# Performance work log

Measured on AMD Instinct MI355X. Metric: run time of the kernel, lower is better.

Reference implementation:

```python
import jax, jax.numpy as jnp
import numpy as np

WH, WW = 16, 16
NUM_HEADS = 16
DIM = 1024
BATCH = 64
SEQ = WH * WW + 1  # 257, includes cls token
NUM_REL = (2 * WH - 1) * (2 * WW - 1) + 3  # 964


def _make_rel_pos_index(wh, ww):
    # BEiT relative position index construction (intended semantics of the torch code)
    coords = np.stack(np.meshgrid(np.arange(wh), np.arange(ww), indexing='ij'))  # [2, wh, ww]
    flat = coords.reshape(2, -1)  # [2, wh*ww]
    rel = flat[:, :, None] - flat[:, None, :]  # [2, N-1, N-1]
    rel = rel.transpose(1, 2, 0).astype(np.int64)
    rel[:, :, 0] += wh - 1
    rel[:, :, 1] += ww - 1
    rel[:, :, 0] *= 2 * ww - 1
    num_rel = (2 * wh - 1) * (2 * ww - 1) + 3
    idx = np.zeros((wh * ww + 1, wh * ww + 1), dtype=np.int32)
    idx[1:, 1:] = rel.sum(-1)
    idx[0, :] = num_rel - 3  # cls-to-token
    idx[:, 0] = num_rel - 2  # token-to-cls
    idx[0, 0] = num_rel - 1  # cls-to-cls
    return idx


def setup_inputs() -> dict:
    key = jax.random.key(0)
    ks = jax.random.split(key, 7)
    return {
        'x': jax.random.normal(ks[0], (BATCH, SEQ, DIM), dtype=jnp.float32),
        'qkv_weight': jax.random.normal(ks[1], (3 * DIM, DIM), dtype=jnp.float32) * 0.02,
        'query_bias': jax.random.normal(ks[2], (DIM,), dtype=jnp.float32) * 0.02,
        'value_bias': jax.random.normal(ks[3], (DIM,), dtype=jnp.float32) * 0.02,
        'rel_pos_bias_table': jax.random.normal(ks[4], (NUM_REL, NUM_HEADS), dtype=jnp.float32) * 0.02,
        'proj_weight': jax.random.normal(ks[5], (DIM, DIM), dtype=jnp.float32) * 0.02,
        'proj_bias': jax.random.normal(ks[6], (DIM,), dtype=jnp.float32) * 0.02,
        'rel_pos_index': jnp.asarray(_make_rel_pos_index(WH, WW)),
    }


def reference(x, qkv_weight, query_bias, value_bias, rel_pos_bias_table,
              proj_weight, proj_bias, rel_pos_index):
    B, N, C = x.shape
    H = rel_pos_bias_table.shape[-1]
    D = qkv_weight.shape[0] // 3 // H
    scale = D ** -0.5
    # qkv bias: (q_bias, zeros, v_bias) as in the torch module
    qkv_bias = jnp.concatenate([query_bias, jnp.zeros_like(value_bias), value_bias])
    qkv = x @ qkv_weight.T + qkv_bias  # [B, N, 3*H*D]
    qkv = qkv.reshape(B, N, 3, H, D).transpose(2, 0, 3, 1, 4)  # [3, B, H, N, D]
    q, k, v = qkv[0] * scale, qkv[1], qkv[2]
    attn = jnp.einsum('bhqd,bhkd->bhqk', q, k)  # [B, H, N, N]
    bias = rel_pos_bias_table[rel_pos_index]  # [N, N, H]
    attn = attn + bias.transpose(2, 0, 1)[None]  # add per-head bias
    attn = jax.nn.softmax(attn, axis=-1)
    out = jnp.einsum('bhqk,bhkd->bhqd', attn, v)  # [B, H, N, D]
    out = out.transpose(0, 2, 1, 3).reshape(B, N, H * D)
    return out @ proj_weight.T + proj_bias
```

## Files before the change

kernel.cpp:

```cpp
#include <hip/hip_runtime.h>


typedef unsigned short u16;
typedef __attribute__((ext_vector_type(8))) short bf16x8;
typedef __attribute__((ext_vector_type(4))) float f32x4;

#define MFMA16(a, b, c) __builtin_amdgcn_mfma_f32_16x16x32_bf16(a, b, c, 0, 0, 0)
#define GLDS16(g, l)                                                           \
  __builtin_amdgcn_global_load_lds(                                            \
      (const __attribute__((address_space(1))) void*)(g),                      \
      (__attribute__((address_space(3))) void*)(l), 16, 0, 0)

#define QOFF 0
#define KOFF 16842752
#define VTOFF 33685504
#define VTP 264

__device__ __forceinline__ u16 f2bf(float f) {
  unsigned u = __builtin_bit_cast(unsigned, f);
  u += 0x7FFFu + ((u >> 16) & 1u);
  return (u16)(u >> 16);
}

__global__ __launch_bounds__(256) void cvt_bf16(const float* __restrict__ in,
                                                u16* __restrict__ out, int n4) {
  int i = blockIdx.x * 256 + threadIdx.x;
  if (i < n4) {
    float4 v = ((const float4*)in)[i];
    uint2 o;
    o.x = (unsigned)f2bf(v.x) | ((unsigned)f2bf(v.y) << 16);
    o.y = (unsigned)f2bf(v.z) | ((unsigned)f2bf(v.w) << 16);
    ((uint2*)out)[i] = o;
  }
}

__global__ __launch_bounds__(256) void bias_pre(const float* __restrict__ tab,
                                                const int* __restrict__ idx,
                                                float* __restrict__ out) {
  int t = blockIdx.x * 256 + threadIdx.x;
  if (t < 66049) {
    int id = idx[t];
    const float* row = tab + (size_t)id * 16;
#pragma unroll
    for (int h = 0; h < 16; h++)
      out[(size_t)h * 66049 + t] = row[h] * 1.4426950408889634f;
  }
}


#define GEMM_PROLOG(M_, K_)                                                    \
  __shared__ __align__(16) u16 As[128 * 32];                                   \
  __shared__ __align__(16) u16 Bs[128 * 32];                                   \
  const int M = (M_), K = (K_);                                                \
  const int tid = threadIdx.x;                                                 \
  const int lane = tid & 63, wave = tid >> 6;                                  \
  const int quad = lane >> 4, l15 = lane & 15;                                 \
  const int wr = (wave >> 1) * 64, wc = (wave & 1) * 64;                       \
  const int m0 = blockIdx.y * 128, n0 = blockIdx.x * 128;                      \
  int ar0 = m0 + (tid >> 2); if (ar0 > M - 1) ar0 = M - 1;                     \
  int ar1 = m0 + 64 + (tid >> 2); if (ar1 > M - 1) ar1 = M - 1;                \
  const u16* pa0 = A + (size_t)ar0 * K + (tid & 3) * 8;                        \
  const u16* pa1 = A + (size_t)ar1 * K + (tid & 3) * 8;                        \
  const u16* pb0 = B + (size_t)(n0 + (tid >> 2)) * K + (tid & 3) * 8;          \
  const u16* pb1 = pb0 + (size_t)64 * K;                                       \
  f32x4 acc[4][4];                                                             \
  _Pragma("unroll") for (int i = 0; i < 4; i++)                                \
  _Pragma("unroll") for (int j = 0; j < 4; j++)                                \
      acc[i][j] = (f32x4){0.f, 0.f, 0.f, 0.f};                                 \
  for (int k0 = 0; k0 < K; k0 += 32) {                                         \
    __syncthreads();                                                           \
    GLDS16(pa0 + k0, As + tid * 8);                                            \
    GLDS16(pa1 + k0, As + 2048 + tid * 8);                                     \
    GLDS16(pb0 + k0, Bs + tid * 8);                                            \
    GLDS16(pb1 + k0, Bs + 2048 + tid * 8);                                     \
    __syncthreads();                                                           \
    bf16x8 af[4], bf[4];                                                       \
    _Pragma("unroll") for (int t = 0; t < 4; t++)                              \
        af[t] = *(const bf16x8*)(As + (wr + t * 16 + l15) * 32 + quad * 8);    \
    _Pragma("unroll") for (int t = 0; t < 4; t++)                              \
        bf[t] = *(const bf16x8*)(Bs + (wc + t * 16 + l15) * 32 + quad * 8);    \
    _Pragma("unroll") for (int i = 0; i < 4; i++)                              \
    _Pragma("unroll") for (int j = 0; j < 4; j++)                              \
        acc[i][j] = MFMA16(af[i], bf[j], acc[i][j]);                           \
  }

__global__ __launch_bounds__(256) void gemm_qkv(
    const u16* __restrict__ A, const u16* __restrict__ B,
    const float* __restrict__ qbias, const float* __restrict__ vbias,
    u16* __restrict__ C) {
  GEMM_PROLOG(16448, 1024)
#pragma unroll
  for (int i = 0; i < 4; i++) {
#pragma unroll
    for (int r = 0; r < 4; r++) {
      int row = m0 + wr + i * 16 + quad * 4 + r;
      if (row < M) {
        unsigned bb = (unsigned)row / 257u;
        unsigned nn = (unsigned)row - bb * 257u;
#pragma unroll
        for (int j = 0; j < 4; j++) {
          int c = n0 + wc + j * 16 + l15;
          int which = c >> 10, rem = c & 1023;
          float bias = (which == 0) ? qbias[rem]
                                    : ((which == 2) ? vbias[rem] : 0.f);
          float v = acc[i][j][r] + bias;
          if (which == 0) v *= 0.18033688011112042f;
          int h = rem >> 6, d = rem & 63;
          size_t dst;
          if (which == 2) {
            dst = (size_t)VTOFF + ((size_t)(bb * 16 + h) * 64 + d) * VTP + nn;
          } else {
            dst = (size_t)which * 16842752 + (size_t)(bb * 16 + h) * 16448 +
                  (size_t)nn * 64 + d;
          }
          C[dst] = f2bf(v);
        }
      }
    }
  }
}

__global__ __launch_bounds__(256) void gemm_proj(
    const u16* __restrict__ A, const u16* __restrict__ B,
    const float* __restrict__ pbias, float* __restrict__ C) {
  GEMM_PROLOG(16448, 1024)
#pragma unroll
  for (int i = 0; i < 4; i++) {
#pragma unroll
    for (int r = 0; r < 4; r++) {
      int row = m0 + wr + i * 16 + quad * 4 + r;
      if (row < M) {
#pragma unroll
        for (int j = 0; j < 4; j++) {
          int c = n0 + wc + j * 16 + l15;
          C[(size_t)row * 1024 + c] = acc[i][j][r] + pbias[c];
        }
      }
    }
  }
}

__global__ __launch_bounds__(256, 3) void attn_fused(
    const u16* __restrict__ qkv, const float* __restrict__ biasT,
    u16* __restrict__ out) {
  __shared__ __align__(16) u16 KVs[96 * 72];
  __shared__ __align__(16) u16 Ps[4 * 16 * 104];
  const int bx = blockIdx.x;
  const int qt = bx % 5, bh = bx / 5;
  const int b = bh >> 4, h = bh & 15;
  const int tid = threadIdx.x, lane = tid & 63, wave = tid >> 6;
  const int quad = lane >> 4, l15 = lane & 15;
  const u16* qg = qkv + QOFF + (size_t)bh * 16448;
  const u16* kg = qkv + KOFF + (size_t)bh * 16448;
  const u16* vtg = qkv + VTOFF + (size_t)bh * (64 * VTP);

  int qra = qt * 64 + wave * 16 + l15;
  if (qra > 256) qra = 256;
  const bf16x8 aq0 = *(const bf16x8*)(qg + (size_t)qra * 64 + quad * 8);
  const bf16x8 aq1 = *(const bf16x8*)(qg + (size_t)qra * 64 + 32 + quad * 8);

  const int qbase = qt * 64 + wave * 16 + quad * 4;
  const float* bb = biasT + (size_t)h * 66049;
  f32x4 s[18];
#pragma unroll
  for (int r = 0; r < 4; r++) {
    int qr = qbase + r;
    if (qr > 256) qr = 256;
    const float* brow = bb + (size_t)qr * 257;
#pragma unroll
    for (int t = 0; t < 18; t++) {
      int kc = t * 16 + l15;
      s[t][r] = (kc < 257) ? brow[kc] : -3e38f;
    }
  }

  const bf16x8 zv = {0, 0, 0, 0, 0, 0, 0, 0};
  for (int ck = 0; ck < 3; ck++) {
    __syncthreads();
#pragma unroll
    for (int it = 0; it < 3; it++) {
      int g = it * 256 + tid;
      int row = g >> 3, col = (g & 7) * 8;
      int gr = ck * 96 + row;
      bf16x8 kv = (gr < 257) ? *(const bf16x8*)(kg + (size_t)gr * 64 + col) : zv;
      *(bf16x8*)(KVs + row * 72 + col) = kv;
    }
    __syncthreads();
#pragma unroll
    for (int nt = 0; nt < 6; nt++) {
      bf16x8 b0 = *(const bf16x8*)(KVs + (nt * 16 + l15) * 72 + quad * 8);
      bf16x8 b1 = *(const bf16x8*)(KVs + (nt * 16 + l15) * 72 + 32 + quad * 8);
      int t = ck * 6 + nt;
      s[t] = MFMA16(aq0, b0, s[t]);
      s[t] = MFMA16(aq1, b1, s[t]);
    }
  }

  float inv[4];
#pragma unroll
  for (int r = 0; r < 4; r++) {
    float m = -3e38f;
#pragma unroll
    for (int t = 0; t < 18; t++) m = fmaxf(m, s[t][r]);
    m = fmaxf(m, __shfl_xor(m, 1));
    m = fmaxf(m, __shfl_xor(m, 2));
    m = fmaxf(m, __shfl_xor(m, 4));
    m = fmaxf(m, __shfl_xor(m, 8));
    float sum = 0.f;
#pragma unroll
    for (int t = 0; t < 18; t++) {
      float p = __builtin_amdgcn_exp2f(s[t][r] - m);
      s[t][r] = p;
      sum += p;
    }
    sum += __shfl_xor(sum, 1);
    sum += __shfl_xor(sum, 2);
    sum += __shfl_xor(sum, 4);
    sum += __shfl_xor(sum, 8);
    inv[r] = 1.f / sum;
  }

  u16* Pw = Ps + wave * (16 * 104);
  f32x4 o[4];
#pragma unroll
  for (int nt = 0; nt < 4; nt++) o[nt] = (f32x4){0.f, 0.f, 0.f, 0.f};
  for (int ck = 0; ck < 3; ck++) {
    __syncthreads();
#pragma unroll
    for (int it = 0; it < 3; it++) {
      int g = it * 256 + tid;
      int row = g / 12, c = (g % 12) * 8;
      bf16x8 v = *(const bf16x8*)(vtg + (size_t)row * VTP + ck * 96 + c);
      *(bf16x8*)(KVs + row * 104 + c) = v;
    }
#pragma unroll
    for (int nt = 0; nt < 6; nt++) {
      int t = ck * 6 + nt;
#pragma unroll
      for (int r = 0; r < 4; r++)
        Pw[(quad * 4 + r) * 104 + nt * 16 + l15] = f2bf(s[t][r]);
    }
    __syncthreads();
#pragma unroll
    for (int ks = 0; ks < 3; ks++) {
      bf16x8 ap = *(const bf16x8*)(Pw + l15 * 104 + ks * 32 + quad * 8);
#pragma unroll
      for (int nt = 0; nt < 4; nt++) {
        bf16x8 bv =
            *(const bf16x8*)(KVs + (nt * 16 + l15) * 104 + ks * 32 + quad * 8);
        o[nt] = MFMA16(ap, bv, o[nt]);
      }
    }
  }

#pragma unroll
  for (int nt = 0; nt < 4; nt++) {
    int d = nt * 16 + l15;
#pragma unroll
    for (int r = 0; r < 4; r++) {
      int qr = qbase + r;
      if (qr < 257)
        out[((size_t)b * 257 + qr) * 1024 + h * 64 + d] =
            f2bf(o[nt][r] * inv[r]);
    }
  }
}

extern "C" void kernel_launch(void* const* d_in, const int* in_sizes, int n_in,
                              void* d_out, int out_size, void* d_ws,
                              size_t ws_size, hipStream_t stream) {
  const float* x = (const float*)d_in[0];
  const float* qkvw = (const float*)d_in[1];
  const float* qb = (const float*)d_in[2];
  const float* vb = (const float*)d_in[3];
  const float* tab = (const float*)d_in[4];
  const float* pw = (const float*)d_in[5];
  const float* pb = (const float*)d_in[6];
  const int* rpi = (const int*)d_in[7];

  char* ws = (char*)d_ws;
  u16* qkvbuf = (u16*)ws;
  u16* xbuf = (u16*)(ws + 101974016);
  float* biasb = (float*)(ws + 135659520);
  u16* qkvwb = (u16*)(ws + 139886656);
  u16* projwb = (u16*)(ws + 146178112);

  cvt_bf16<<<16448, 256, 0, stream>>>(x, xbuf, 4210688);
  cvt_bf16<<<3072, 256, 0, stream>>>(qkvw, qkvwb, 786432);
  cvt_bf16<<<1024, 256, 0, stream>>>(pw, projwb, 262144);
  bias_pre<<<259, 256, 0, stream>>>(tab, rpi, biasb);
  gemm_qkv<<<dim3(24, 129), 256, 0, stream>>>(xbuf, qkvwb, qb, vb, qkvbuf);
  attn_fused<<<5120, 256, 0, stream>>>(qkvbuf, biasb, xbuf);
  gemm_proj<<<dim3(8, 129), 256, 0, stream>>>(xbuf, projwb, pb, (float*)d_out);
}
```

Baseline: 469.6 us.

## Double GEMM K-tile to 64 with XOR-swizzled LDS layout

Shared GEMM prolog now stages a 128x64 K-slab per iteration instead of 128x32, halving the number of barrier pairs and load rounds per K. The LDS layout applies an XOR swizzle on 16-byte chunks by row so the wider rows do not cause bank conflicts on the fragment reads. This doubles LDS use per block, which may reduce occupancy.

New measurement: 493.2 us. 1.05x slower.

```diff
diff --git a/kernel.cpp b/kernel.cpp
--- a/kernel.cpp
+++ b/kernel.cpp
@@ -49,39 +49,50 @@
 
 
 #define GEMM_PROLOG(M_, K_)                                                    \
-  __shared__ __align__(16) u16 As[128 * 32];                                   \
-  __shared__ __align__(16) u16 Bs[128 * 32];                                   \
+  __shared__ __align__(16) u16 As[128 * 64];                                   \
+  __shared__ __align__(16) u16 Bs[128 * 64];                                   \
   const int M = (M_), K = (K_);                                                \
   const int tid = threadIdx.x;                                                 \
   const int lane = tid & 63, wave = tid >> 6;                                  \
   const int quad = lane >> 4, l15 = lane & 15;                                 \
   const int wr = (wave >> 1) * 64, wc = (wave & 1) * 64;                       \
   const int m0 = blockIdx.y * 128, n0 = blockIdx.x * 128;                      \
-  int ar0 = m0 + (tid >> 2); if (ar0 > M - 1) ar0 = M - 1;                     \
-  int ar1 = m0 + 64 + (tid >> 2); if (ar1 > M - 1) ar1 = M - 1;                \
-  const u16* pa0 = A + (size_t)ar0 * K + (tid & 3) * 8;                        \
-  const u16* pa1 = A + (size_t)ar1 * K + (tid & 3) * 8;                        \
-  const u16* pb0 = B + (size_t)(n0 + (tid >> 2)) * K + (tid & 3) * 8;          \
-  const u16* pb1 = pb0 + (size_t)64 * K;                                       \
+  const int srow = tid >> 3;                      \
+  const int sg = (tid & 7) ^ (srow & 7);          \
+  const u16* pa[4];                                                            \
+  const u16* pb[4];                                                            \
+  _Pragma("unroll") for (int c = 0; c < 4; c++) {                              \
+    int arow = m0 + c * 32 + srow; if (arow > M - 1) arow = M - 1;             \
+    pa[c] = A + (size_t)arow * K + sg * 8;                                     \
+    pb[c] = B + (size_t)(n0 + c * 32 + srow) * K + sg * 8;                     \
+  }                                                                            \
   f32x4 acc[4][4];                                                             \
   _Pragma("unroll") for (int i = 0; i < 4; i++)                                \
   _Pragma("unroll") for (int j = 0; j < 4; j++)                                \
       acc[i][j] = (f32x4){0.f, 0.f, 0.f, 0.f};                                 \
-  for (int k0 = 0; k0 < K; k0 += 32) {                                         \
+  for (int k0 = 0; k0 < K; k0 += 64) {                                         \
     __syncthreads();                                                           \
-    GLDS16(pa0 + k0, As + tid * 8);                                            \
-    GLDS16(pa1 + k0, As + 2048 + tid * 8);                                     \
-    GLDS16(pb0 + k0, Bs + tid * 8);                                            \
-    GLDS16(pb1 + k0, Bs + 2048 + tid * 8);                                     \
+    _Pragma("unroll") for (int c = 0; c < 4; c++) {                            \
+      GLDS16(pa[c] + k0, As + (c * 256 + tid) * 8);                            \
+      GLDS16(pb[c] + k0, Bs + (c * 256 + tid) * 8);                            \
+    }                                                                          \
     __syncthreads();                                                           \
-    bf16x8 af[4], bf[4];                                                       \
-    _Pragma("unroll") for (int t = 0; t < 4; t++)                              \
-        af[t] = *(const bf16x8*)(As + (wr + t * 16 + l15) * 32 + quad * 8);    \
-    _Pragma("unroll") for (int t = 0; t < 4; t++)                              \
-        bf[t] = *(const bf16x8*)(Bs + (wc + t * 16 + l15) * 32 + quad * 8);    \
-    _Pragma("unroll") for (int i = 0; i < 4; i++)                              \
-    _Pragma("unroll") for (int j = 0; j < 4; j++)                              \
-        acc[i][j] = MFMA16(af[i], bf[j], acc[i][j]);                           \
+    _Pragma("unroll") for (int kk = 0; kk < 2; kk++) {                         \
+      bf16x8 af[4], bf[4];                                                     \
+      _Pragma("unroll") for (int t = 0; t < 4; t++) {                          \
+        int r = wr + t * 16 + l15;                                             \
+        af[t] = *(const bf16x8*)(As + r * 64 +                                 \
+                                 (((kk * 4 + quad) ^ (r & 7)) * 8));           \
+      }                                                                        \
+      _Pragma("unroll") for (int t = 0; t < 4; t++) {                          \
+        int r = wc + t * 16 + l15;                                             \
+        bf[t] = *(const bf16x8*)(Bs + r * 64 +                                 \
+                                 (((kk * 4 + quad) ^ (r & 7)) * 8));           \
+      }                                                                        \
+      _Pragma("unroll") for (int i = 0; i < 4; i++)                            \
+      _Pragma("unroll") for (int j = 0; j < 4; j++)                            \
+          acc[i][j] = MFMA16(af[i], bf[j], acc[i][j]);                         \
+    }                                                                          \
   }
 
 __global__ __launch_bounds__(256) void gemm_qkv(
```
